# Kernel optimization log

Measured on AMD Instinct MI355X. Metric: run time of the kernel, lower is better.

## Reference

```python
import jax, jax.numpy as jnp
import numpy as np

N_NODES = 100000
N_EDGES = 3200000
IN_F, HID_F, OUT_F = 6, 32, 3


def setup_inputs() -> dict:
    key = jax.random.key(0)
    k_feat, k_src, k_dst, k_w1, k_w2 = jax.random.split(key, 5)
    features = jax.random.normal(k_feat, (N_NODES, IN_F), dtype=jnp.float32)
    src = jax.random.randint(k_src, (N_EDGES,), 0, N_NODES, dtype=jnp.int32)
    dst = jax.random.randint(k_dst, (N_EDGES,), 0, N_NODES, dtype=jnp.int32)
    # Glorot-style weights for the two customConv layers
    W1 = jax.random.normal(k_w1, (IN_F, HID_F), dtype=jnp.float32) / np.sqrt(IN_F)
    b1 = jnp.zeros((HID_F,), dtype=jnp.float32)
    W2 = jax.random.normal(k_w2, (HID_F, OUT_F), dtype=jnp.float32) / np.sqrt(HID_F)
    b2 = jnp.zeros((OUT_F,), dtype=jnp.float32)
    return {"features": features, "src": src, "dst": dst,
            "W1": W1, "b1": b1, "W2": W2, "b2": b2}


def _custom_conv(src, dst, h, W, b):
    """DGL-GraphConv-style layer: mean-aggregate src->dst, then linear.
    h: [N, F_in]; returns [N, F_out]."""
    n = h.shape[0]
    # gather source features along edges, scatter-add to destinations
    msg_sum = jax.ops.segment_sum(h[src], dst, num_segments=n)  # [N, F_in]
    deg = jax.ops.segment_sum(jnp.ones_like(dst, dtype=h.dtype), dst,
                              num_segments=n)                    # [N]
    agg = msg_sum / jnp.maximum(deg, 1.0)[:, None]               # mean over in-neighbors
    return agg @ W + b


def reference(features, src, dst, W1, b1, W2, b2):
    x = _custom_conv(src, dst, features, W1, b1)  # [N, 32]
    x = jax.nn.relu(x)                            # activation inside customConv
    x = _custom_conv(src, dst, x, W2, b2)         # [N, 3]
    return x
```

## Files before the change

kernel.cpp:

```cpp
#include <hip/hip_runtime.h>


#define IN_F 6
#define HID_F 32
#define OUT_F 3

#define NPB 256
#define NPB_SHIFT 8
#define NBMAX 512
#define CAPB 9728
#define CHUNK 8192
#define EPT 8
#define SRC_BITS 17
#define SRC_MASK ((1u << SRC_BITS) - 1)

__global__ void k_zero(int* __restrict__ cursor, int nB) {
    for (int i = threadIdx.x; i < nB; i += blockDim.x) cursor[i] = 0;
}

__global__ __launch_bounds__(1024)
void k_scatter(const int* __restrict__ src, const int* __restrict__ dst,
               int nB, int* __restrict__ cursor_g,
               unsigned* __restrict__ packed, int nE) {
    __shared__ int      hist[NBMAX];
    __shared__ int      base_l[NBMAX];
    __shared__ int      base_g[NBMAX];
    __shared__ int      cur[NBMAX];
    __shared__ unsigned sorted_l[CHUNK];
    __shared__ unsigned short bkt_l[CHUNK];

    const int tid = threadIdx.x;
    int e0 = blockIdx.x * CHUNK;
    int e1 = min(e0 + CHUNK, nE);
    int cnt = e1 - e0;

    for (int b = tid; b < nB; b += blockDim.x) hist[b] = 0;
    __syncthreads();

    int dr[EPT];
#pragma unroll
    for (int k = 0; k < EPT; ++k) {
        int e = e0 + tid + k * 1024;
        dr[k] = (e < e1) ? dst[e] : -1;
    }
#pragma unroll
    for (int k = 0; k < EPT; ++k)
        if (dr[k] >= 0) atomicAdd(&hist[dr[k] >> NPB_SHIFT], 1);
    __syncthreads();

    if (tid < nB) base_l[tid] = hist[tid];
    __syncthreads();
    for (int off = 1; off < nB; off <<= 1) {
        int v = 0;
        if (tid < nB) {
            v = base_l[tid];
            if (tid >= off) v += base_l[tid - off];
        }
        __syncthreads();
        if (tid < nB) base_l[tid] = v;
        __syncthreads();
    }

    int h_r = 0, ex_r = 0;
    if (tid < nB) {
        h_r  = hist[tid];
        ex_r = base_l[tid] - h_r;
        base_g[tid] = h_r ? atomicAdd(&cursor_g[tid], h_r) : 0;
        cur[tid] = ex_r;
    }
    __syncthreads();
    if (tid < nB) base_l[tid] = ex_r;
    __syncthreads();

#pragma unroll
    for (int k = 0; k < EPT; ++k) {
        int e = e0 + tid + k * 1024;
        if (e < e1) {
            int d = dr[k];
            int b = d >> NPB_SHIFT;
            unsigned rec = ((unsigned)(d & (NPB - 1)) << SRC_BITS) | (unsigned)src[e];
            int p = atomicAdd(&cur[b], 1);
            sorted_l[p] = rec;
            bkt_l[p] = (unsigned short)b;
        }
    }
    __syncthreads();

    for (int i = tid; i < cnt; i += blockDim.x) {
        int b = bkt_l[i];
        int rel = base_g[b] + (i - base_l[b]);
        if (rel < CAPB) packed[(size_t)b * CAPB + rel] = sorted_l[i];
    }
}

__global__ __launch_bounds__(1024)
void k_sl1(unsigned* __restrict__ packed, const int* __restrict__ cursor_g,
           const float* __restrict__ feat,
           const float* __restrict__ W1, const float* __restrict__ b1,
           const float* __restrict__ W2,
           float4* __restrict__ g4, int* __restrict__ offv, int* __restrict__ cntv,
           int nN) {
    __shared__ int      hist[NPB];
    __shared__ int      base[NPB];
    __shared__ int      cur[NPB];
    __shared__ unsigned sorted[CAPB];
    __shared__ float    sW1[IN_F * HID_F];
    __shared__ float    sb1[HID_F];
    __shared__ float    sW2[HID_F * OUT_F];

    const int tid = threadIdx.x;
    int b = blockIdx.x;
    int ecnt = min(cursor_g[b], CAPB);
    unsigned* ep = packed + (size_t)b * CAPB;

    for (int i = tid; i < IN_F * HID_F; i += blockDim.x)  sW1[i] = W1[i];
    for (int i = tid; i < HID_F; i += blockDim.x)         sb1[i] = b1[i];
    for (int i = tid; i < HID_F * OUT_F; i += blockDim.x) sW2[i] = W2[i];
    if (tid < NPB) hist[tid] = 0;
    __syncthreads();

    for (int i = tid; i < ecnt; i += blockDim.x)
        atomicAdd(&hist[ep[i] >> SRC_BITS], 1);
    __syncthreads();

    if (tid < NPB) base[tid] = hist[tid];
    __syncthreads();
    for (int off = 1; off < NPB; off <<= 1) {
        int v = 0;
        if (tid < NPB) {
            v = base[tid];
            if (tid >= off) v += base[tid - off];
        }
        __syncthreads();
        if (tid < NPB) base[tid] = v;
        __syncthreads();
    }

    int n0 = b << NPB_SHIFT;
    int h_r = 0, ex_r = 0;
    if (tid < NPB) {
        h_r  = hist[tid];
        ex_r = base[tid] - h_r;
        cur[tid] = ex_r;
        int n = n0 + tid;
        if (n < nN) { offv[n] = b * CAPB + ex_r; cntv[n] = h_r; }
    }
    __syncthreads();
    if (tid < NPB) base[tid] = ex_r;
    __syncthreads();

    for (int i = tid; i < ecnt; i += blockDim.x) {
        unsigned p = ep[i];
        int dl = (int)(p >> SRC_BITS);
        int pos = atomicAdd(&cur[dl], 1);
        sorted[pos] = p & SRC_MASK;
    }
    __syncthreads();

    for (int i = tid; i < ecnt; i += blockDim.x) ep[i] = sorted[i];

    int node = tid >> 2;
    int sub  = tid & 3;
    int n    = n0 + node;
    bool live = (n < nN);

    float s0 = 0.f, s1 = 0.f, s2 = 0.f, s3 = 0.f, s4 = 0.f, s5 = 0.f;
    int st = 0, c = 0;
    if (live) { st = base[node]; c = hist[node]; }

    for (int i = st + sub; i < st + c; i += 4) {
        unsigned s = sorted[i];
        const float* f = feat + (size_t)s * IN_F;
        float2 f01 = *reinterpret_cast<const float2*>(f + 0);
        float2 f23 = *reinterpret_cast<const float2*>(f + 2);
        float2 f45 = *reinterpret_cast<const float2*>(f + 4);
        s0 += f01.x; s1 += f01.y; s2 += f23.x;
        s3 += f23.y; s4 += f45.x; s5 += f45.y;
    }
    s0 += __shfl_xor(s0, 1); s0 += __shfl_xor(s0, 2);
    s1 += __shfl_xor(s1, 1); s1 += __shfl_xor(s1, 2);
    s2 += __shfl_xor(s2, 1); s2 += __shfl_xor(s2, 2);
    s3 += __shfl_xor(s3, 1); s3 += __shfl_xor(s3, 2);
    s4 += __shfl_xor(s4, 1); s4 += __shfl_xor(s4, 2);
    s5 += __shfl_xor(s5, 1); s5 += __shfl_xor(s5, 2);

    float inv = 1.0f / fmaxf((float)c, 1.0f);
    float a0 = s0 * inv, a1 = s1 * inv, a2 = s2 * inv;
    float a3 = s3 * inv, a4 = s4 * inv, a5 = s5 * inv;

    float g0 = 0.f, g1 = 0.f, g2 = 0.f;
    int j0 = sub * (HID_F / 4);
#pragma unroll
    for (int jj = 0; jj < HID_F / 4; ++jj) {
        int j = j0 + jj;
        float t = sb1[j];
        t = fmaf(a0, sW1[0 * HID_F + j], t);
        t = fmaf(a1, sW1[1 * HID_F + j], t);
        t = fmaf(a2, sW1[2 * HID_F + j], t);
        t = fmaf(a3, sW1[3 * HID_F + j], t);
        t = fmaf(a4, sW1[4 * HID_F + j], t);
        t = fmaf(a5, sW1[5 * HID_F + j], t);
        t = fmaxf(t, 0.0f);
        g0 = fmaf(t, sW2[j * OUT_F + 0], g0);
        g1 = fmaf(t, sW2[j * OUT_F + 1], g1);
        g2 = fmaf(t, sW2[j * OUT_F + 2], g2);
    }
    g0 += __shfl_xor(g0, 1); g0 += __shfl_xor(g0, 2);
    g1 += __shfl_xor(g1, 1); g1 += __shfl_xor(g1, 2);
    g2 += __shfl_xor(g2, 1); g2 += __shfl_xor(g2, 2);

    if (live && sub == 0) g4[n] = make_float4(g0, g1, g2, 0.0f);
}

__global__ void k_l2(const unsigned* __restrict__ csr, const int* __restrict__ offv,
                     const int* __restrict__ cntv, const float4* __restrict__ g4,
                     const float* __restrict__ b2, float* __restrict__ out, int nN) {
    int gid  = blockIdx.x * blockDim.x + threadIdx.x;
    int node = gid >> 2;
    int sub  = gid & 3;
    if (node >= nN) return;

    int off = offv[node], c = cntv[node];
    const unsigned* row = csr + off;

    float s0 = 0.f, s1 = 0.f, s2 = 0.f;
    for (int i = sub; i < c; i += 4) {
        float4 ga = g4[row[i]];
        s0 += ga.x; s1 += ga.y; s2 += ga.z;
    }
    s0 += __shfl_xor(s0, 1); s0 += __shfl_xor(s0, 2);
    s1 += __shfl_xor(s1, 1); s1 += __shfl_xor(s1, 2);
    s2 += __shfl_xor(s2, 1); s2 += __shfl_xor(s2, 2);

    if (sub == 0) {
        float inv = 1.0f / fmaxf((float)c, 1.0f);
        out[(size_t)node * OUT_F + 0] = s0 * inv + b2[0];
        out[(size_t)node * OUT_F + 1] = s1 * inv + b2[1];
        out[(size_t)node * OUT_F + 2] = s2 * inv + b2[2];
    }
}

__global__ void scatter1(const int* __restrict__ src, const int* __restrict__ dst,
                         const float* __restrict__ feat,
                         float* __restrict__ acc1, float* __restrict__ deg, int nE) {
    int e = blockIdx.x * blockDim.x + threadIdx.x;
    if (e >= nE) return;
    int s = src[e], d = dst[e];
    const float* f = feat + (size_t)s * IN_F;
    float* a = acc1 + (size_t)d * IN_F;
    float2 f01 = *reinterpret_cast<const float2*>(f + 0);
    float2 f23 = *reinterpret_cast<const float2*>(f + 2);
    float2 f45 = *reinterpret_cast<const float2*>(f + 4);
    atomicAdd(a + 0, f01.x); atomicAdd(a + 1, f01.y); atomicAdd(a + 2, f23.x);
    atomicAdd(a + 3, f23.y); atomicAdd(a + 4, f45.x); atomicAdd(a + 5, f45.y);
    atomicAdd(deg + d, 1.0f);
}

__global__ void node_mlp(float* __restrict__ acc1, const float* __restrict__ deg,
                         const float* __restrict__ W1, const float* __restrict__ b1,
                         const float* __restrict__ W2, int nN) {
    __shared__ float sW1[IN_F * HID_F];
    __shared__ float sb1[HID_F];
    __shared__ float sW2[HID_F * OUT_F];
    for (int i = threadIdx.x; i < IN_F * HID_F; i += blockDim.x)  sW1[i] = W1[i];
    for (int i = threadIdx.x; i < HID_F; i += blockDim.x)         sb1[i] = b1[i];
    for (int i = threadIdx.x; i < HID_F * OUT_F; i += blockDim.x) sW2[i] = W2[i];
    __syncthreads();
    int n = blockIdx.x * blockDim.x + threadIdx.x;
    if (n >= nN) return;
    float inv = 1.0f / fmaxf(deg[n], 1.0f);
    float a[IN_F];
    float* row = acc1 + (size_t)n * IN_F;
#pragma unroll
    for (int i = 0; i < IN_F; ++i) a[i] = row[i] * inv;
    float g0 = 0.f, g1 = 0.f, g2 = 0.f;
#pragma unroll
    for (int j = 0; j < HID_F; ++j) {
        float t = sb1[j];
#pragma unroll
        for (int i = 0; i < IN_F; ++i) t = fmaf(a[i], sW1[i * HID_F + j], t);
        t = fmaxf(t, 0.0f);
        g0 = fmaf(t, sW2[j * OUT_F + 0], g0);
        g1 = fmaf(t, sW2[j * OUT_F + 1], g1);
        g2 = fmaf(t, sW2[j * OUT_F + 2], g2);
    }
    row[0] = g0; row[1] = g1; row[2] = g2;
}

__global__ void scatter2(const int* __restrict__ src, const int* __restrict__ dst,
                         const float* __restrict__ g, float* __restrict__ acc2, int nE) {
    int e = blockIdx.x * blockDim.x + threadIdx.x;
    if (e >= nE) return;
    int s = src[e], d = dst[e];
    const float* gs = g + (size_t)s * IN_F;
    float* a = acc2 + (size_t)d * OUT_F;
    float2 g01 = *reinterpret_cast<const float2*>(gs);
    atomicAdd(a + 0, g01.x); atomicAdd(a + 1, g01.y); atomicAdd(a + 2, gs[2]);
}

__global__ void finalize(const float* __restrict__ acc2, const float* __restrict__ deg,
                         const float* __restrict__ b2, float* __restrict__ out, int nN) {
    int n = blockIdx.x * blockDim.x + threadIdx.x;
    if (n >= nN) return;
    float inv = 1.0f / fmaxf(deg[n], 1.0f);
    out[(size_t)n * OUT_F + 0] = acc2[(size_t)n * OUT_F + 0] * inv + b2[0];
    out[(size_t)n * OUT_F + 1] = acc2[(size_t)n * OUT_F + 1] * inv + b2[1];
    out[(size_t)n * OUT_F + 2] = acc2[(size_t)n * OUT_F + 2] * inv + b2[2];
}

extern "C" void kernel_launch(void* const* d_in, const int* in_sizes, int n_in,
                              void* d_out, int out_size, void* d_ws, size_t ws_size,
                              hipStream_t stream) {
    const float* feat = (const float*)d_in[0];
    const int*   src  = (const int*)d_in[1];
    const int*   dst  = (const int*)d_in[2];
    const float* W1   = (const float*)d_in[3];
    const float* b1   = (const float*)d_in[4];
    const float* W2   = (const float*)d_in[5];
    const float* b2   = (const float*)d_in[6];
    float* out = (float*)d_out;

    const int nN = in_sizes[0] / IN_F;
    const int nE = in_sizes[1];

    int nB = (nN + NPB - 1) >> NPB_SHIFT;
    int nC = (nE + CHUNK - 1) / CHUNK;

    size_t off_g4     = 0;
    size_t off_offv   = off_g4 + (size_t)nN * sizeof(float4);
    size_t off_cntv   = off_offv + (size_t)nN * sizeof(int);
    size_t off_cursor = off_cntv + (size_t)nN * sizeof(int);
    size_t off_packed = (off_cursor + (size_t)nB * sizeof(int) + 255) & ~(size_t)255;
    size_t need_fast  = off_packed + (size_t)nB * CAPB * sizeof(unsigned);

    bool fast = (ws_size >= need_fast) &&
                (nN <= (int)(SRC_MASK + 1)) &&
                (nB <= NBMAX) &&
                (nE / nB <= CAPB - 1500);

    if (fast) {
        float4*   g4     = (float4*)((char*)d_ws + off_g4);
        int*      offv   = (int*)((char*)d_ws + off_offv);
        int*      cntv   = (int*)((char*)d_ws + off_cntv);
        int*      cursor = (int*)((char*)d_ws + off_cursor);
        unsigned* packed = (unsigned*)((char*)d_ws + off_packed);

        k_zero<<<1, 512, 0, stream>>>(cursor, nB);
        k_scatter<<<nC, 1024, 0, stream>>>(src, dst, nB, cursor, packed, nE);
        k_sl1<<<nB, 1024, 0, stream>>>(packed, cursor, feat, W1, b1, W2,
                                       g4, offv, cntv, nN);
        k_l2<<<(nN * 4 + 255) / 256, 256, 0, stream>>>(packed, offv, cntv, g4,
                                                       b2, out, nN);
    } else {
        float* deg  = (float*)d_ws;
        float* acc1 = deg + nN;
        float* acc2 = acc1 + (size_t)nN * IN_F;
        const int TB = 256;
        int eblocks = (nE + TB - 1) / TB;
        int nblocks = (nN + TB - 1) / TB;
        hipMemsetAsync(d_ws, 0, (size_t)nN * 10 * sizeof(float), stream);
        scatter1<<<eblocks, TB, 0, stream>>>(src, dst, feat, acc1, deg, nE);
        node_mlp<<<nblocks, TB, 0, stream>>>(acc1, deg, W1, b1, W2, nN);
        scatter2<<<eblocks, TB, 0, stream>>>(src, dst, acc1, acc2, nE);
        finalize<<<nblocks, TB, 0, stream>>>(acc2, deg, b2, out, nN);
    }
}
```

Baseline: 79.09 us.

## Pad features to 8 floats, use wave scans, smaller scatter chunks, register-held edges

Adds a kernel that pads the 6-float node features to two float4 per node, so the layer-1 gather does two 16-byte loads instead of three 8-byte loads. The block-level Hillis-Steele scans in the scatter and sort kernels become wave shuffle scans, which need far fewer __syncthreads. The scatter kernel now uses 512 threads over 4096-edge chunks and preloads src into registers. k_sl1 keeps its packed edges in registers across the histogram and placement passes instead of reading global memory twice. The cost is an extra kernel launch, a padded feature copy (double the feature footprint), and higher register pressure from the ERMAX=10 preload.

```diff
diff --git a/kernel.cpp b/kernel.cpp
--- a/kernel.cpp
+++ b/kernel.cpp
@@ -9,16 +9,39 @@
 #define NPB_SHIFT 8
 #define NBMAX 512
 #define CAPB 9728
-#define CHUNK 8192
-#define EPT 8
+#define CHUNK 4096
+#define SCT 512
+#define EPT (CHUNK/SCT)
+#define ERMAX 10
+#define SENT 0xFFFFFFFFu
 #define SRC_BITS 17
 #define SRC_MASK ((1u << SRC_BITS) - 1)
 
+__device__ __forceinline__ int wave_incl_scan(int v, int lane) {
+#pragma unroll
+    for (int d = 1; d < 64; d <<= 1) {
+        int u = __shfl_up(v, d);
+        if (lane >= d) v += u;
+    }
+    return v;
+}
+
 __global__ void k_zero(int* __restrict__ cursor, int nB) {
     for (int i = threadIdx.x; i < nB; i += blockDim.x) cursor[i] = 0;
 }
 
-__global__ __launch_bounds__(1024)
+__global__ void k_pad(const float* __restrict__ feat, float4* __restrict__ feat8, int nN) {
+    int n = blockIdx.x * blockDim.x + threadIdx.x;
+    if (n >= nN) return;
+    const float* f = feat + (size_t)n * IN_F;
+    float2 f01 = *reinterpret_cast<const float2*>(f + 0);
+    float2 f23 = *reinterpret_cast<const float2*>(f + 2);
+    float2 f45 = *reinterpret_cast<const float2*>(f + 4);
+    feat8[2 * n + 0] = make_float4(f01.x, f01.y, f23.x, f23.y);
+    feat8[2 * n + 1] = make_float4(f45.x, f45.y, 0.0f, 0.0f);
+}
+
+__global__ __launch_bounds__(SCT)
 void k_scatter(const int* __restrict__ src, const int* __restrict__ dst,
                int nB, int* __restrict__ cursor_g,
                unsigned* __restrict__ packed, int nE) {
@@ -26,59 +49,57 @@
     __shared__ int      base_l[NBMAX];
     __shared__ int      base_g[NBMAX];
     __shared__ int      cur[NBMAX];
+    __shared__ int      wsum[SCT / 64];
     __shared__ unsigned sorted_l[CHUNK];
     __shared__ unsigned short bkt_l[CHUNK];
 
-    const int tid = threadIdx.x;
+    const int tid  = threadIdx.x;
+    const int lane = tid & 63;
+    const int wid  = tid >> 6;
     int e0 = blockIdx.x * CHUNK;
     int e1 = min(e0 + CHUNK, nE);
     int cnt = e1 - e0;
 
-    for (int b = tid; b < nB; b += blockDim.x) hist[b] = 0;
-    __syncthreads();
-
-    int dr[EPT];
+    for (int b = tid; b < nB; b += SCT) hist[b] = 0;
+
+    int dr[EPT], sr[EPT];
 #pragma unroll
     for (int k = 0; k < EPT; ++k) {
-        int e = e0 + tid + k * 1024;
+        int e = e0 + tid + k * SCT;
         dr[k] = (e < e1) ? dst[e] : -1;
-    }
+        sr[k] = (e < e1) ? src[e] : 0;
+    }
+    __syncthreads();
+
 #pragma unroll
     for (int k = 0; k < EPT; ++k)
         if (dr[k] >= 0) atomicAdd(&hist[dr[k] >> NPB_SHIFT], 1);
     __syncthreads();
 
-    if (tid < nB) base_l[tid] = hist[tid];
-    __syncthreads();
-    for (int off = 1; off < nB; off <<= 1) {
-        int v = 0;
-        if (tid < nB) {
-            v = base_l[tid];
-            if (tid >= off) v += base_l[tid - off];
-        }
-        __syncthreads();
-        if (tid < nB) base_l[tid] = v;
-        __syncthreads();
-    }
-
-    int h_r = 0, ex_r = 0;
+    int h = (tid < nB) ? hist[tid] : 0;
+    int incl = wave_incl_scan(h, lane);
+    if (lane == 63) wsum[wid] = incl;
+    __syncthreads();
+    if (wid == 0) {
+        int t = (lane < SCT / 64) ? wsum[lane] : 0;
+        t = wave_incl_scan(t, lane);
+        if (lane < SCT / 64) wsum[lane] = t;
+    }
+    __syncthreads();
+    int ex = incl + (wid ? wsum[wid - 1] : 0) - h;
     if (tid < nB) {
-        h_r  = hist[tid];
-        ex_r = base_l[tid] - h_r;
-        base_g[tid] = h_r ? atomicAdd(&cursor_g[tid], h_r) : 0;
-        cur[tid] = ex_r;
-    }
-    __syncthreads();
-    if (tid < nB) base_l[tid] = ex_r;
+        base_g[tid] = h ? atomicAdd(&cursor_g[tid], h) : 0;
+        base_l[tid] = ex;
+        cur[tid]    = ex;
+    }
     __syncthreads();
 
 #pragma unroll
     for (int k = 0; k < EPT; ++k) {
-        int e = e0 + tid + k * 1024;
-        if (e < e1) {
+        if (dr[k] >= 0) {
             int d = dr[k];
             int b = d >> NPB_SHIFT;
-            unsigned rec = ((unsigned)(d & (NPB - 1)) << SRC_BITS) | (unsigned)src[e];
+            unsigned rec = ((unsigned)(d & (NPB - 1)) << SRC_BITS) | (unsigned)sr[k];
             int p = atomicAdd(&cur[b], 1);
             sorted_l[p] = rec;
             bkt_l[p] = (unsigned short)b;
@@ -86,7 +107,7 @@
     }
     __syncthreads();
 
-    for (int i = tid; i < cnt; i += blockDim.x) {
+    for (int i = tid; i < cnt; i += SCT) {
         int b = bkt_l[i];
         int rel = base_g[b] + (i - base_l[b]);
         if (rel < CAPB) packed[(size_t)b * CAPB + rel] = sorted_l[i];
@@ -95,7 +116,7 @@
 
 __global__ __launch_bounds__(1024)
 void k_sl1(unsigned* __restrict__ packed, const int* __restrict__ cursor_g,
-           const float* __restrict__ feat,
+           const float4* __restrict__ feat8,
            const float* __restrict__ W1, const float* __restrict__ b1,
            const float* __restrict__ W2,
            float4* __restrict__ g4, int* __restrict__ offv, int* __restrict__ cntv,
@@ -103,12 +124,15 @@
     __shared__ int      hist[NPB];
     __shared__ int      base[NPB];
     __shared__ int      cur[NPB];
+    __shared__ int      wsum[16];
     __shared__ unsigned sorted[CAPB];
     __shared__ float    sW1[IN_F * HID_F];
     __shared__ float    sb1[HID_F];
     __shared__ float    sW2[HID_F * OUT_F];
 
-    const int tid = threadIdx.x;
+    const int tid  = threadIdx.x;
+    const int lane = tid & 63;
+    const int wid  = tid >> 6;
     int b = blockIdx.x;
     int ecnt = min(cursor_g[b], CAPB);
     unsigned* ep = packed + (size_t)b * CAPB;
@@ -117,43 +141,48 @@
     for (int i = tid; i < HID_F; i += blockDim.x)         sb1[i] = b1[i];
     for (int i = tid; i < HID_F * OUT_F; i += blockDim.x) sW2[i] = W2[i];
     if (tid < NPB) hist[tid] = 0;
-    __syncthreads();
-
-    for (int i = tid; i < ecnt; i += blockDim.x)
-        atomicAdd(&hist[ep[i] >> SRC_BITS], 1);
-    __syncthreads();
-
-    if (tid < NPB) base[tid] = hist[tid];
-    __syncthreads();
-    for (int off = 1; off < NPB; off <<= 1) {
-        int v = 0;
-        if (tid < NPB) {
-            v = base[tid];
-            if (tid >= off) v += base[tid - off];
+
+    unsigned er[ERMAX];
+#pragma unroll
+    for (int k = 0; k < ERMAX; ++k) {
+        int i = tid + k * 1024;
+        er[k] = (i < ecnt) ? ep[i] : SENT;
+    }
+    __syncthreads();
+
+#pragma unroll
+    for (int k = 0; k < ERMAX; ++k)
+        if (er[k] != SENT) atomicAdd(&hist[er[k] >> SRC_BITS], 1);
+    __syncthreads();
+
+    int h = (tid < NPB) ? hist[tid] : 0;
+    int incl = wave_incl_scan(h, lane);
+    if (lane == 63) wsum[wid] = incl;
+    __syncthreads();
+    if (wid == 0) {
+        int t = (lane < 16) ? wsum[lane] : 0;
+        t = wave_incl_scan(t, lane);
+        if (lane < 16) wsum[lane] = t;
+    }
+    __syncthreads();
+    int n0 = b << NPB_SHIFT;
+    int ex = incl + (wid ? wsum[wid - 1] : 0) - h;
+    if (tid < NPB) {
+        base[tid] = ex;
+        cur[tid]  = ex;
+        int n = n0 + tid;
+        if (n < nN) { offv[n] = b * CAPB + ex; cntv[n] = h; }
+    }
+    __syncthreads();
+
+#pragma unroll
+    for (int k = 0; k < ERMAX; ++k) {
+        if (er[k] != SENT) {
+            unsigned p = er[k];
+            int dl = (int)(p >> SRC_BITS);
+            int pos = atomicAdd(&cur[dl], 1);
+            sorted[pos] = p & SRC_MASK;
         }
-        __syncthreads();
-        if (tid < NPB) base[tid] = v;
-        __syncthreads();
-    }
-
-    int n0 = b << NPB_SHIFT;
-    int h_r = 0, ex_r = 0;
-    if (tid < NPB) {
-        h_r  = hist[tid];
-        ex_r = base[tid] - h_r;
-        cur[tid] = ex_r;
-        int n = n0 + tid;
-        if (n < nN) { offv[n] = b * CAPB + ex_r; cntv[n] = h_r; }
-    }
-    __syncthreads();
-    if (tid < NPB) base[tid] = ex_r;
-    __syncthreads();
-
-    for (int i = tid; i < ecnt; i += blockDim.x) {
-        unsigned p = ep[i];
-        int dl = (int)(p >> SRC_BITS);
-        int pos = atomicAdd(&cur[dl], 1);
-        sorted[pos] = p & SRC_MASK;
     }
     __syncthreads();
 
@@ -170,12 +199,11 @@
 
     for (int i = st + sub; i < st + c; i += 4) {
         unsigned s = sorted[i];
-        const float* f = feat + (size_t)s * IN_F;
-        float2 f01 = *reinterpret_cast<const float2*>(f + 0);
-        float2 f23 = *reinterpret_cast<const float2*>(f + 2);
-        float2 f45 = *reinterpret_cast<const float2*>(f + 4);
-        s0 += f01.x; s1 += f01.y; s2 += f23.x;
-        s3 += f23.y; s4 += f45.x; s5 += f45.y;
+        const float4* f8 = feat8 + 2 * (size_t)s;
+        float4 fa = f8[0];
+        float4 fb = f8[1];
+        s0 += fa.x; s1 += fa.y; s2 += fa.z;
+        s3 += fa.w; s4 += fb.x; s5 += fb.y;
     }
     s0 += __shfl_xor(s0, 1); s0 += __shfl_xor(s0, 2);
     s1 += __shfl_xor(s1, 1); s1 += __shfl_xor(s1, 2);
@@ -326,7 +354,8 @@
     int nB = (nN + NPB - 1) >> NPB_SHIFT;
     int nC = (nE + CHUNK - 1) / CHUNK;
 
-    size_t off_g4     = 0;
+    size_t off_feat8  = 0;
+    size_t off_g4     = off_feat8 + (size_t)nN * 2 * sizeof(float4);
     size_t off_offv   = off_g4 + (size_t)nN * sizeof(float4);
     size_t off_cntv   = off_offv + (size_t)nN * sizeof(int);
     size_t off_cursor = off_cntv + (size_t)nN * sizeof(int);
@@ -339,6 +368,7 @@
                 (nE / nB <= CAPB - 1500);
 
     if (fast) {
+        float4*   feat8  = (float4*)((char*)d_ws + off_feat8);
         float4*   g4     = (float4*)((char*)d_ws + off_g4);
         int*      offv   = (int*)((char*)d_ws + off_offv);
         int*      cntv   = (int*)((char*)d_ws + off_cntv);
@@ -346,8 +376,9 @@
         unsigned* packed = (unsigned*)((char*)d_ws + off_packed);
 
         k_zero<<<1, 512, 0, stream>>>(cursor, nB);
-        k_scatter<<<nC, 1024, 0, stream>>>(src, dst, nB, cursor, packed, nE);
-        k_sl1<<<nB, 1024, 0, stream>>>(packed, cursor, feat, W1, b1, W2,
+        k_pad<<<(nN + 255) / 256, 256, 0, stream>>>(feat, feat8, nN);
+        k_scatter<<<nC, SCT, 0, stream>>>(src, dst, nB, cursor, packed, nE);
+        k_sl1<<<nB, 1024, 0, stream>>>(packed, cursor, feat8, W1, b1, W2,
                                        g4, offv, cntv, nN);
         k_l2<<<(nN * 4 + 255) / 256, 256, 0, stream>>>(packed, offv, cntv, g4,
                                                        b2, out, nN);
```

New measurement: 91.73 us. 16.0% more time.
